# Kernel tuning notes

Hardware: AMD Instinct MI355X
Metric: run time of the kernel (lower is better)

## Reference

```python
import jax, jax.numpy as jnp
import numpy as np

HID = 128
MAX_NODES = 100000
MAX_EDGES = 300000
EVT_LEN = 4096
NUM_NODE = 20000
NUM_EDGE = 320000
# EVENT_TYPE_ID_MAP: pad=0 start=1 end=2 node-add=3 node-delete=4 edge-add=5 edge-delete=6
NODE_ADD, NODE_DEL = 3, 4


def time_encode(t, time_w, time_b):
    # TimeEncoder: cos(Linear(1 -> hidden)(t))
    return jnp.cos(t[..., None] * time_w + time_b)


def gru_cell(x, h, w_ih, w_hh, b_ih, b_hh):
    gi = x @ w_ih.T + b_ih
    gh = h @ w_hh.T + b_hh
    i_r, i_z, i_n = jnp.split(gi, 3, axis=-1)
    h_r, h_z, h_n = jnp.split(gh, 3, axis=-1)
    r = jax.nn.sigmoid(i_r + h_r)
    z = jax.nn.sigmoid(i_z + h_z)
    n = jnp.tanh(i_n + r * h_n)
    return (1.0 - z) * n + z * h


def setup_inputs() -> dict:
    key = jax.random.key(0)
    ks = jax.random.split(key, 32)
    H = HID
    s = 0.05
    inp = {}
    inp["event_type_ids"] = jax.random.randint(ks[0], (EVT_LEN,), 0, 7)
    inp["src_ids"] = jax.random.randint(ks[1], (EVT_LEN,), 0, MAX_NODES)
    inp["src_mask"] = (jax.random.uniform(ks[2], (EVT_LEN,)) > 0.3).astype(jnp.float32)
    inp["dst_ids"] = jax.random.randint(ks[3], (EVT_LEN,), 0, MAX_NODES)
    inp["dst_mask"] = (jax.random.uniform(ks[4], (EVT_LEN,)) > 0.3).astype(jnp.float32)
    inp["event_edge_ids"] = jax.random.randint(ks[5], (EVT_LEN,), 0, MAX_EDGES)
    inp["event_embeddings"] = jax.random.normal(ks[6], (EVT_LEN, H), dtype=jnp.float32)
    inp["event_mask"] = (jax.random.uniform(ks[7], (EVT_LEN,)) > 0.2).astype(jnp.float32)
    inp["event_timestamps"] = jax.random.uniform(ks[8], (EVT_LEN,)) * 100.0
    inp["node_ids"] = jax.random.randint(ks[9], (NUM_NODE,), 0, MAX_NODES)
    inp["edge_ids"] = jax.random.randint(ks[10], (NUM_EDGE,), 0, MAX_EDGES)
    inp["edge_index"] = jax.random.randint(ks[11], (2, NUM_EDGE), 0, NUM_NODE)
    inp["time"] = 100
    # persistent-buffer state
    inp["memory"] = jax.random.normal(ks[12], (MAX_NODES, H), dtype=jnp.float32) * s
    inp["last_update"] = jax.random.uniform(ks[13], (MAX_EDGES,)) * 50.0
    inp["node_features"] = jax.random.normal(ks[14], (MAX_NODES, H), dtype=jnp.float32) * s
    inp["edge_features"] = jax.random.normal(ks[15], (MAX_EDGES, H), dtype=jnp.float32) * s
    # TimeEncoder params (Linear(1, H))
    inp["time_w"] = jax.random.normal(ks[16], (H,), dtype=jnp.float32) * s
    inp["time_b"] = jax.random.normal(ks[17], (H,), dtype=jnp.float32) * s
    # GRUCell(5H -> H)
    inp["gru_w_ih"] = jax.random.normal(ks[18], (3 * H, 5 * H), dtype=jnp.float32) * s
    inp["gru_w_hh"] = jax.random.normal(ks[19], (3 * H, H), dtype=jnp.float32) * s
    inp["gru_b_ih"] = jax.random.normal(ks[20], (3 * H,), dtype=jnp.float32) * s
    inp["gru_b_hh"] = jax.random.normal(ks[21], (3 * H,), dtype=jnp.float32) * s
    # TransformerConv(H, H, heads=1, edge_dim=2H)
    inp["wq"] = jax.random.normal(ks[22], (H, H), dtype=jnp.float32) * s
    inp["bq"] = jax.random.normal(ks[23], (H,), dtype=jnp.float32) * s
    inp["wk"] = jax.random.normal(ks[24], (H, H), dtype=jnp.float32) * s
    inp["bk"] = jax.random.normal(ks[25], (H,), dtype=jnp.float32) * s
    inp["wv"] = jax.random.normal(ks[26], (H, H), dtype=jnp.float32) * s
    inp["bv"] = jax.random.normal(ks[27], (H,), dtype=jnp.float32) * s
    inp["we"] = jax.random.normal(ks[28], (H, 2 * H), dtype=jnp.float32) * s  # lin_edge, no bias
    inp["wskip"] = jax.random.normal(ks[29], (H, H), dtype=jnp.float32) * s
    inp["bskip"] = jax.random.normal(ks[30], (H,), dtype=jnp.float32) * s
    return inp


def reference(event_type_ids, src_ids, src_mask, dst_ids, dst_mask, event_edge_ids,
              event_embeddings, event_mask, event_timestamps, node_ids, edge_ids,
              edge_index, time, memory, last_update, node_features, edge_features,
              time_w, time_b, gru_w_ih, gru_w_hh, gru_b_ih, gru_b_hh,
              wq, bq, wk, bk, wv, bv, we, wskip, bskip):
    H = HID
    # ---- message() ----
    L = event_type_ids.shape[0]
    type_embs = jnp.broadcast_to(event_type_ids[:, None].astype(memory.dtype), (L, H))
    src_embs = memory[src_ids] * src_mask[:, None]
    dst_embs = memory[dst_ids] * dst_mask[:, None]
    edge_last = last_update[event_edge_ids]
    rel_ts = event_timestamps - edge_last * dst_mask
    is_node_ev = ((event_type_ids == NODE_ADD) | (event_type_ids == NODE_DEL)).astype(event_timestamps.dtype)
    ts_emb = time_encode(event_timestamps * is_node_ev + rel_ts * dst_mask, time_w, time_b) * event_mask[:, None]
    src_msgs = jnp.concatenate([type_embs, src_embs, dst_embs, ts_emb, event_embeddings], axis=1) * event_mask[:, None]
    dst_msgs = jnp.concatenate([type_embs, dst_embs, src_embs, ts_emb, event_embeddings], axis=1) * dst_mask[:, None]
    # ---- agg_message(): scatter-mean over node ids ----
    def agg(msgs, ids):
        s = jax.ops.segment_sum(msgs, ids, num_segments=MAX_NODES)
        c = jax.ops.segment_sum(jnp.ones((msgs.shape[0],), msgs.dtype), ids, num_segments=MAX_NODES)
        return s / jnp.maximum(c, 1.0)[:, None]
    agg_src = agg(src_msgs, src_ids)
    agg_dst = agg(dst_msgs, dst_ids)
    # ---- GRU memory update on unique ids ----
    # torch: memory[cat(uniq_src, uniq_dst)] = rnn(...); reads use pre-update memory,
    # dst writes come after src writes so they override on overlap. Duplicate ids in
    # src_ids carry identical per-id values, so scatter-set is equivalent to unique().
    new_src = gru_cell(agg_src[src_ids], memory[src_ids], gru_w_ih, gru_w_hh, gru_b_ih, gru_b_hh)
    new_dst = gru_cell(agg_dst[dst_ids], memory[dst_ids], gru_w_ih, gru_w_hh, gru_b_ih, gru_b_hh)
    memory = memory.at[src_ids].set(new_src)
    memory = memory.at[dst_ids].set(new_dst)
    # ---- edge attributes ----
    rel_t = time - last_update[edge_ids]
    rel_t_embs = time_encode(rel_t, time_w, time_b)
    edge_attr = jnp.concatenate([rel_t_embs, edge_features[edge_ids]], axis=-1)  # (E, 2H)
    # ---- TransformerConv (heads=1, concat, root_weight) ----
    x = node_features[node_ids] + memory[node_ids]  # (N, H)
    src, dst = edge_index[0], edge_index[1]
    q = x @ wq.T + bq
    k = x @ wk.T + bk
    v = x @ wv.T + bv
    e = edge_attr @ we.T  # lin_edge (no bias)
    alpha = jnp.sum(q[dst] * (k[src] + e), axis=-1) / jnp.sqrt(jnp.asarray(H, x.dtype))
    amax = jax.ops.segment_max(alpha, dst, num_segments=x.shape[0])
    ex = jnp.exp(alpha - amax[dst])
    denom = jax.ops.segment_sum(ex, dst, num_segments=x.shape[0])
    p = ex / jnp.maximum(denom[dst], 1e-16)
    out = jax.ops.segment_sum(p[:, None] * (v[src] + e), dst, num_segments=x.shape[0])
    return out + x @ wskip.T + bskip
```

## Files before the change

### kernel.cpp

```cpp
#include <hip/hip_runtime.h>
#include <math.h>

#define HID   128
#define MAXN  100000
#define MAXE  300000
#define EVT   4096
#define NNODE 20000
#define NEDGE 320000

typedef unsigned short u16;
typedef __attribute__((ext_vector_type(8))) short bf16x8;
typedef __attribute__((ext_vector_type(4))) float f32x4;

#define OFF_WIHB      0u
#define OFF_WHHB      491520u
#define OFF_WEB       589824u
#define OFF_WALLB     655360u
#define OFF_BALL      851968u
#define BASE2         855040u
#define OFF_REP_SRC   (BASE2 + 0u)
#define OFF_REP_DST   (BASE2 + 400128u)
#define OFF_CNT_SRC   (BASE2 + 800256u)
#define OFF_CNT_DST   (BASE2 + 1200384u)
#define OFF_SUM_SRC   (BASE2 + 1600512u)
#define OFF_SUM_DST   (BASE2 + 12086272u)
#define OFF_XGB       (BASE2 + 22572032u)
#define OFF_HG        (BASE2 + 33057792u)
#define OFF_HGB       (BASE2 + 37252096u)
#define OFF_GI        (BASE2 + 39349248u)
#define OFF_GH        (BASE2 + 51932160u)
#define OFF_NEWMEM    (BASE2 + 64515072u)
#define OFF_XB        (BASE2 + 0u)
#define OFF_QKVSE     (BASE2 + 5120000u)
#define OFF_KVB       (BASE2 + 66560000u)
#define OFF_DEG       (BASE2 + 76800000u)
#define OFF_OFFS      (BASE2 + 76880128u)
#define OFF_CURSOR    (BASE2 + 76960256u)
#define OFF_BSUM      (BASE2 + 77040384u)
#define OFF_SORTED    (BASE2 + 77041664u)
#define OFF_SACCB     (BASE2 + 78321664u)

__device__ __forceinline__ float sigmoidf_(float x) { return 1.f / (1.f + __expf(-x)); }
__device__ __forceinline__ u16 f2b(float f) {
    unsigned u = __float_as_uint(f);
    unsigned r = (u + 0x7fffu + ((u >> 16) & 1u)) >> 16;
    return (u16)r;
}
__device__ __forceinline__ float b2f(unsigned h) { return __uint_as_float(h << 16); }

__global__ void k_prep(const float* __restrict__ w_ih, const float* __restrict__ w_hh,
                       const float* __restrict__ we,
                       const float* __restrict__ wq, const float* __restrict__ wk_,
                       const float* __restrict__ wv, const float* __restrict__ wskip,
                       const float* __restrict__ bq, const float* __restrict__ bk,
                       const float* __restrict__ bv, const float* __restrict__ bskip,
                       u16* __restrict__ w_ih_b, u16* __restrict__ w_hh_b,
                       u16* __restrict__ we_b, u16* __restrict__ Wallb,
                       float* __restrict__ ball, int* __restrict__ deg) {
    int b = blockIdx.x, t = threadIdx.x;
    if (b < 960) {
        int i = b * 256 + t;
        w_ih_b[i] = f2b(w_ih[i]);
        return;
    }
    b -= 960;
    if (b < 192) {
        int i = b * 256 + t;
        w_hh_b[i] = f2b(w_hh[i]);
        return;
    }
    b -= 192;
    if (b < 128) {
        int i = b * 256 + t;
        we_b[i] = f2b(we[i]);
        return;
    }
    b -= 128;
    if (b < 79) {
        int i = b * 256 + t;
        if (i < NNODE) deg[i] = 0;
        return;
    }
    b -= 79;
    int idx = b * 256 + t;
    int row = idx >> 7;
    int k = idx & 127;
    float v;
    if (row < 128)      v = wq[row * 128 + k];
    else if (row < 256) v = wk_[(row - 128) * 128 + k];
    else if (row < 384) v = wv[(row - 256) * 128 + k];
    else if (row < 512) v = wskip[(row - 384) * 128 + k];
    else {
        int j = row - 512;
        float a = 0.f;
        for (int t2 = 0; t2 < 128; t2++) a += wq[t2 * 128 + k] * we[t2 * 256 + j];
        v = a;
    }
    Wallb[row * 128 + k] = f2b(v);
    if (k == 0) {
        float bb;
        if (row < 128)      bb = bq[row];
        else if (row < 256) bb = bk[row - 128];
        else if (row < 384) bb = bv[row - 256];
        else if (row < 512) bb = bskip[row - 384];
        else { int j = row - 512; float a = 0.f; for (int t2 = 0; t2 < 128; t2++) a += bq[t2] * we[t2 * 256 + j]; bb = a; }
        ball[row] = bb;
    }
}

__global__ void k_zero(char* __restrict__ base) {
    const int NFF = 50016;
    const int NZ  = 1360736;
    uint4 ff = make_uint4(0xFFFFFFFFu, 0xFFFFFFFFu, 0xFFFFFFFFu, 0xFFFFFFFFu);
    uint4 zz = make_uint4(0u, 0u, 0u, 0u);
    int idx = blockIdx.x * blockDim.x + threadIdx.x;
    int stride = gridDim.x * blockDim.x;
    uint4* pff = (uint4*)base;
    uint4* pzz = (uint4*)(base + 800256);
    for (int i = idx; i < NFF; i += stride) pff[i] = ff;
    for (int i = idx; i < NZ; i += stride) pzz[i] = zz;
}

__global__ void k_tables_deg(const int* __restrict__ src_ids, const int* __restrict__ dst_ids,
                             unsigned* rep_src, unsigned* rep_dst, int* cnt_src, int* cnt_dst,
                             const int* __restrict__ eidx, int* __restrict__ deg) {
    int b = blockIdx.x, t = threadIdx.x;
    if (b < 16) {
        int i = b * 256 + t;
        if (i >= EVT) return;
        int s = src_ids[i], d = dst_ids[i];
        atomicMin(&rep_src[s], (unsigned)i);
        atomicAdd(&cnt_src[s], 1);
        atomicMin(&rep_dst[d], (unsigned)i);
        atomicAdd(&cnt_dst[d], 1);
    } else {
        int j = (b - 16) * 256 + t;
        if (j >= NEDGE) return;
        atomicAdd(&deg[eidx[NEDGE + j]], 1);
    }
}

__global__ void k_message(const int* __restrict__ et_ids, const int* __restrict__ src_ids,
                          const float* __restrict__ src_mask, const int* __restrict__ dst_ids,
                          const float* __restrict__ dst_mask, const int* __restrict__ ev_eids,
                          const float* __restrict__ ev_emb, const float* __restrict__ ev_mask,
                          const float* __restrict__ ev_ts, const float* __restrict__ memory,
                          const float* __restrict__ last_update, const float* __restrict__ time_w,
                          const float* __restrict__ time_b, const unsigned* __restrict__ rep_src,
                          const unsigned* __restrict__ rep_dst, const int* __restrict__ cnt_src,
                          const int* __restrict__ cnt_dst, float* sum_src, float* sum_dst) {
    int i = blockIdx.x;
    int c = threadIdx.x;
    int et = et_ids[i];
    float sm = src_mask[i], dm = dst_mask[i], em = ev_mask[i], ts = ev_ts[i];
    int sid = src_ids[i], did = dst_ids[i], eid = ev_eids[i];
    float isnode = (et == 3 || et == 4) ? 1.f : 0.f;
    float rel = ts - last_update[eid] * dm;
    float tval = ts * isnode + rel * dm;
    float tse = __cosf(tval * time_w[c] + time_b[c]) * em;
    float typ = (float)et;
    float sv = memory[(size_t)sid * HID + c] * sm;
    float dv = memory[(size_t)did * HID + c] * dm;
    float ev = ev_emb[(size_t)i * HID + c];
    float* ps = sum_src + (size_t)rep_src[sid] * 640;
    if (cnt_src[sid] == 1) {
        ps[c] = typ * em; ps[128 + c] = sv * em; ps[256 + c] = dv * em;
        ps[384 + c] = tse * em; ps[512 + c] = ev * em;
    } else {
        atomicAdd(ps + c, typ * em);
        atomicAdd(ps + 128 + c, sv * em);
        atomicAdd(ps + 256 + c, dv * em);
        atomicAdd(ps + 384 + c, tse * em);
        atomicAdd(ps + 512 + c, ev * em);
    }
    float* pd = sum_dst + (size_t)rep_dst[did] * 640;
    if (cnt_dst[did] == 1) {
        pd[c] = typ * dm; pd[128 + c] = dv * dm; pd[256 + c] = sv * dm;
        pd[384 + c] = tse * dm; pd[512 + c] = ev * dm;
    } else {
        atomicAdd(pd + c, typ * dm);
        atomicAdd(pd + 128 + c, dv * dm);
        atomicAdd(pd + 256 + c, sv * dm);
        atomicAdd(pd + 384 + c, tse * dm);
        atomicAdd(pd + 512 + c, ev * dm);
    }
}

__global__ void k_build(const int* __restrict__ src_ids, const int* __restrict__ dst_ids,
                        const unsigned* __restrict__ rep_src, const unsigned* __restrict__ rep_dst,
                        const int* __restrict__ cnt_src, const int* __restrict__ cnt_dst,
                        const float* __restrict__ sum_src, const float* __restrict__ sum_dst,
                        const float* __restrict__ memory, u16* __restrict__ Xgb,
                        float* __restrict__ Hg, u16* __restrict__ Hgb) {
    int r = blockIdx.x, y = blockIdx.y, t = threadIdx.x;
    if (y == 5) {
        int id = (r < EVT) ? src_ids[r] : dst_ids[r - EVT];
        float v = memory[(size_t)id * HID + t];
        Hg[(size_t)r * HID + t] = v;
        Hgb[(size_t)r * HID + t] = f2b(v);
        return;
    }
    int c = y * 128 + t;
    float v;
    if (r < EVT) {
        int id = src_ids[r];
        int cnt = cnt_src[id]; if (cnt < 1) cnt = 1;
        v = sum_src[(size_t)rep_src[id] * 640 + c] / (float)cnt;
    } else {
        int id = dst_ids[r - EVT];
        int cnt = cnt_dst[id]; if (cnt < 1) cnt = 1;
        v = sum_dst[(size_t)rep_dst[id] * 640 + c] / (float)cnt;
    }
    Xgb[(size_t)r * 640 + c] = f2b(v);
}

__device__ __forceinline__ void gemm_tile(const u16* __restrict__ A, const u16* __restrict__ W,
                                          const float* __restrict__ bias, float* __restrict__ C,
                                          u16* __restrict__ KVb, int M, int N, int K, int acc,
                                          u16* Als, u16* Wls) {
    int tid = threadIdx.x;
    int bm = blockIdx.x * 128, bn = blockIdx.y * 128;
    int wave = tid >> 6, lane = tid & 63;
    int wm = (wave & 1) * 64, wn = (wave >> 1) * 64;
    int l15 = lane & 15, quad = lane >> 4;
    f32x4 accf[4][4] = {};
    for (int k0 = 0; k0 < K; k0 += 32) {
#pragma unroll
        for (int h = 0; h < 2; ++h) {
            int ch = tid + h * 256;
            int row = ch >> 2, kc = (ch & 3) * 8;
            int gr = bm + row;
            float4 av = make_float4(0.f, 0.f, 0.f, 0.f);
            if (gr < M) av = *(const float4*)(A + (size_t)gr * K + k0 + kc);
            *(float4*)&Als[row * 40 + kc] = av;
            int wr = bn + row;
            float4 wv_ = *(const float4*)(W + (size_t)wr * K + k0 + kc);
            *(float4*)&Wls[row * 40 + kc] = wv_;
        }
        __syncthreads();
        bf16x8 af[4], bfr[4];
#pragma unroll
        for (int r = 0; r < 4; ++r)
            af[r] = *(const bf16x8*)&Als[(wm + r * 16 + l15) * 40 + quad * 8];
#pragma unroll
        for (int c2 = 0; c2 < 4; ++c2)
            bfr[c2] = *(const bf16x8*)&Wls[(wn + c2 * 16 + l15) * 40 + quad * 8];
#pragma unroll
        for (int r = 0; r < 4; ++r)
#pragma unroll
            for (int c2 = 0; c2 < 4; ++c2)
                accf[r][c2] = __builtin_amdgcn_mfma_f32_16x16x32_bf16(af[r], bfr[c2], accf[r][c2], 0, 0, 0);
        __syncthreads();
    }
#pragma unroll
    for (int r = 0; r < 4; ++r) {
#pragma unroll
        for (int c2 = 0; c2 < 4; ++c2) {
            int ncol = bn + wn + c2 * 16 + l15;
            float bv = bias ? bias[ncol] : 0.f;
#pragma unroll
            for (int reg = 0; reg < 4; ++reg) {
                int mrow = bm + wm + r * 16 + quad * 4 + reg;
                if (mrow >= M) continue;
                float v = accf[r][c2][reg] + bv;
                if (KVb && ncol >= 128 && ncol < 384) {
                    KVb[(size_t)mrow * 256 + (ncol - 128)] = f2b(v);
                } else {
                    if (acc) v += C[(size_t)mrow * N + ncol];
                    C[(size_t)mrow * N + ncol] = v;
                }
            }
        }
    }
}

__global__ __launch_bounds__(256) void k_gemm_mfma(const u16* __restrict__ A,
                                                   const u16* __restrict__ W,
                                                   const float* __restrict__ bias,
                                                   float* __restrict__ C,
                                                   u16* __restrict__ KVb,
                                                   int M, int N, int K, int acc) {
    __shared__ u16 Als[128 * 40];
    __shared__ u16 Wls[128 * 40];
    gemm_tile(A, W, bias, C, KVb, M, N, K, acc, Als, Wls);
}

__global__ __launch_bounds__(256) void k_gemm_dual(const u16* __restrict__ A0, const u16* __restrict__ W0,
                                                   const float* __restrict__ b0, float* __restrict__ C0,
                                                   const u16* __restrict__ A1, const u16* __restrict__ W1,
                                                   const float* __restrict__ b1, float* __restrict__ C1) {
    __shared__ u16 Als[128 * 40];
    __shared__ u16 Wls[128 * 40];
    if (blockIdx.z == 0) gemm_tile(A0, W0, b0, C0, nullptr, 2 * EVT, 384, 640, 0, Als, Wls);
    else                 gemm_tile(A1, W1, b1, C1, nullptr, 2 * EVT, 384, 128, 0, Als, Wls);
}

__global__ void k_gru_scatter(const float* __restrict__ Gi, const float* __restrict__ Gh,
                              const float* __restrict__ Hg, const int* __restrict__ src_ids,
                              const int* __restrict__ dst_ids, const unsigned* __restrict__ rep_dst,
                              float* __restrict__ memory) {
    int r = blockIdx.x, c = threadIdx.x;
    const float* gi = Gi + (size_t)r * 384;
    const float* gh = Gh + (size_t)r * 384;
    float rg = sigmoidf_(gi[c] + gh[c]);
    float z  = sigmoidf_(gi[128 + c] + gh[128 + c]);
    float n  = tanhf(gi[256 + c] + rg * gh[256 + c]);
    float h0 = Hg[(size_t)r * HID + c];
    float h  = (1.f - z) * n + z * h0;
    if (r < EVT) {
        int sid = src_ids[r];
        if (rep_dst[sid] == 0xFFFFFFFFu) memory[(size_t)sid * HID + c] = h;
    } else {
        int did = dst_ids[r - EVT];
        memory[(size_t)did * HID + c] = h;
    }
}

__global__ void k_x(const int* __restrict__ node_ids, const float* __restrict__ nf,
                    const float* __restrict__ memory, u16* __restrict__ Xb) {
    int p = blockIdx.x, c = threadIdx.x;
    int nid = node_ids[p];
    Xb[(size_t)p * HID + c] = f2b(nf[(size_t)nid * HID + c] + memory[(size_t)nid * HID + c]);
}

__global__ __launch_bounds__(1024) void k_scan_one(const int* __restrict__ deg,
                                                   int* __restrict__ offs, int* __restrict__ cursor) {
    __shared__ int wsum[16];
    int t = threadIdx.x, lane = t & 63, w = t >> 6;
    int carry = 0;
    for (int base = 0; base < NNODE; base += 1024) {
        int i = base + t;
        int v = (i < NNODE) ? deg[i] : 0;
        int x = v;
#pragma unroll
        for (int d = 1; d < 64; d <<= 1) { int y = __shfl_up(x, d, 64); if (lane >= d) x += y; }
        if (lane == 63) wsum[w] = x;
        __syncthreads();
        int add = 0, tot = 0;
        for (int k2 = 0; k2 < 16; ++k2) { int s = wsum[k2]; if (k2 < w) add += s; tot += s; }
        if (i < NNODE) { int e = carry + add + x - v; offs[i] = e; cursor[i] = e; }
        carry += tot;
        __syncthreads();
    }
    if (t == 0) offs[NNODE] = NEDGE;
}

__global__ void k_sortscat(const int* __restrict__ eidx, int* __restrict__ cursor,
                           int* __restrict__ sorted) {
    int j = blockIdx.x * blockDim.x + threadIdx.x;
    if (j >= NEDGE) return;
    int d = eidx[NEDGE + j];
    int pos = atomicAdd(&cursor[d], 1);
    sorted[pos] = j;
}

__global__ __launch_bounds__(256) void k_node(const float* __restrict__ QK,
        const u16* __restrict__ KVb, const int* __restrict__ offs,
        const int* __restrict__ sorted, const int* __restrict__ eidx,
        const int* __restrict__ edge_ids, const float* __restrict__ last_update,
        const float* __restrict__ time_w, const float* __restrict__ time_b,
        const float* __restrict__ ef, const int* __restrict__ tptr,
        float* __restrict__ out, u16* __restrict__ saccb) {
    int wave = threadIdx.x >> 6, lane = threadIdx.x & 63;
    int n = blockIdx.x * 4 + wave;
    int c = 2 * lane;
    const float* base = QK + (size_t)n * 768;
    float2 qd   = *(const float2*)(base + c);
    float2 skip = *(const float2*)(base + 384 + c);
    float2 qet  = *(const float2*)(base + 512 + c);
    float2 qef  = *(const float2*)(base + 640 + c);
    float2 tw   = *(const float2*)(time_w + c);
    float2 tb   = *(const float2*)(time_b + c);
    float tf = (float)(*tptr);
    int start = offs[n], end = offs[n + 1];
    int deg = end - start;
    if (deg == 0) {
        *(float2*)(out + (size_t)n * HID + c) = skip;
        *(unsigned*)(saccb + (size_t)n * 256 + c) = 0u;
        *(unsigned*)(saccb + (size_t)n * 256 + 128 + c) = 0u;
        return;
    }
    float m = -1e30f, l_ = 0.f;
    float va0 = 0.f, va1 = 0.f, s00 = 0.f, s01 = 0.f, s10 = 0.f, s11 = 0.f;
    for (int cb = start; cb < end; cb += 64) {
        int cnt = end - cb; if (cnt > 64) cnt = 64;
        int s_l = 0, eid_l = 0; float rt_l = 0.f;
        if (lane < cnt) {
            int j = sorted[cb + lane];
            s_l = eidx[j];
            eid_l = edge_ids[j];
            rt_l = tf - last_update[eid_l];
        }
        for (int e0 = 0; e0 < cnt; e0 += 4) {
            float pv[4], cv0[4], cv1[4], vx[4], vy[4], ex[4], ey[4];
#pragma unroll
            for (int i = 0; i < 4; ++i) {
                int idx = e0 + i;
                int sel = (idx < cnt) ? idx : e0;
                int s   = __shfl(s_l, sel, 64);
                int eid = __shfl(eid_l, sel, 64);
                float rt = __shfl(rt_l, sel, 64);
                unsigned kvp = *(const unsigned*)(KVb + (size_t)s * 256 + c);
                unsigned vvp = *(const unsigned*)(KVb + (size_t)s * 256 + 128 + c);
                float2 ev = *(const float2*)(ef + (size_t)eid * HID + c);
                float k0f = b2f(kvp & 0xffffu), k1f = b2f(kvp >> 16);
                vx[i] = b2f(vvp & 0xffffu); vy[i] = b2f(vvp >> 16);
                cv0[i] = __cosf(rt * tw.x + tb.x);
                cv1[i] = __cosf(rt * tw.y + tb.y);
                ex[i] = ev.x; ey[i] = ev.y;
                pv[i] = qd.x * k0f + qd.y * k1f + qet.x * cv0[i] + qet.y * cv1[i]
                      + qef.x * ev.x + qef.y * ev.y;
            }
#pragma unroll
            for (int msk = 32; msk > 0; msk >>= 1) {
#pragma unroll
                for (int i = 0; i < 4; ++i) pv[i] += __shfl_xor(pv[i], msk, 64);
            }
            float al[4];
#pragma unroll
            for (int i = 0; i < 4; ++i)
                al[i] = (e0 + i < cnt) ? pv[i] * 0.08838834764831845f : -1e30f;
            float gm = fmaxf(fmaxf(al[0], al[1]), fmaxf(al[2], al[3]));
            if (gm > m) {
                float fac = __expf(m - gm);
                l_ *= fac; va0 *= fac; va1 *= fac;
                s00 *= fac; s01 *= fac; s10 *= fac; s11 *= fac;
                m = gm;
            }
#pragma unroll
            for (int i = 0; i < 4; ++i) {
                float w = __expf(al[i] - m);
                l_ += w;
                va0 += w * vx[i]; va1 += w * vy[i];
                s00 += w * cv0[i]; s01 += w * cv1[i];
                s10 += w * ex[i]; s11 += w * ey[i];
            }
        }
    }
    float inv = 1.f / fmaxf(l_, 1e-16f);
    float2 o; o.x = va0 * inv + skip.x; o.y = va1 * inv + skip.y;
    *(float2*)(out + (size_t)n * HID + c) = o;
    unsigned p0 = (unsigned)f2b(s00 * inv) | ((unsigned)f2b(s01 * inv) << 16);
    unsigned p1 = (unsigned)f2b(s10 * inv) | ((unsigned)f2b(s11 * inv) << 16);
    *(unsigned*)(saccb + (size_t)n * 256 + c) = p0;
    *(unsigned*)(saccb + (size_t)n * 256 + 128 + c) = p1;
}

extern "C" void kernel_launch(void* const* d_in, const int* in_sizes, int n_in,
                              void* d_out, int out_size, void* d_ws, size_t ws_size,
                              hipStream_t stream) {
    const int*   et_ids        = (const int*)d_in[0];
    const int*   src_ids       = (const int*)d_in[1];
    const float* src_mask      = (const float*)d_in[2];
    const int*   dst_ids       = (const int*)d_in[3];
    const float* dst_mask      = (const float*)d_in[4];
    const int*   ev_eids       = (const int*)d_in[5];
    const float* ev_emb        = (const float*)d_in[6];
    const float* ev_mask       = (const float*)d_in[7];
    const float* ev_ts         = (const float*)d_in[8];
    const int*   node_ids      = (const int*)d_in[9];
    const int*   edge_ids      = (const int*)d_in[10];
    const int*   edge_index    = (const int*)d_in[11];
    const int*   tptr          = (const int*)d_in[12];
    float*       memory        = (float*)d_in[13];
    const float* last_update   = (const float*)d_in[14];
    const float* node_features = (const float*)d_in[15];
    const float* edge_features = (const float*)d_in[16];
    const float* time_w        = (const float*)d_in[17];
    const float* time_b        = (const float*)d_in[18];
    const float* w_ih          = (const float*)d_in[19];
    const float* w_hh          = (const float*)d_in[20];
    const float* b_ih          = (const float*)d_in[21];
    const float* b_hh          = (const float*)d_in[22];
    const float* wq            = (const float*)d_in[23];
    const float* bq            = (const float*)d_in[24];
    const float* wk            = (const float*)d_in[25];
    const float* bk            = (const float*)d_in[26];
    const float* wv            = (const float*)d_in[27];
    const float* bv            = (const float*)d_in[28];
    const float* we            = (const float*)d_in[29];
    const float* wskip         = (const float*)d_in[30];
    const float* bskip         = (const float*)d_in[31];
    float* out = (float*)d_out;
    char*  wsb = (char*)d_ws;

    u16*   w_ih_b  = (u16*)(wsb + OFF_WIHB);
    u16*   w_hh_b  = (u16*)(wsb + OFF_WHHB);
    u16*   we_b    = (u16*)(wsb + OFF_WEB);
    u16*   Wallb   = (u16*)(wsb + OFF_WALLB);
    float* ball    = (float*)(wsb + OFF_BALL);
    unsigned* rep_src = (unsigned*)(wsb + OFF_REP_SRC);
    unsigned* rep_dst = (unsigned*)(wsb + OFF_REP_DST);
    int*   cnt_src = (int*)(wsb + OFF_CNT_SRC);
    int*   cnt_dst = (int*)(wsb + OFF_CNT_DST);
    float* sum_src = (float*)(wsb + OFF_SUM_SRC);
    float* sum_dst = (float*)(wsb + OFF_SUM_DST);
    u16*   Xgb     = (u16*)(wsb + OFF_XGB);
    float* Hg      = (float*)(wsb + OFF_HG);
    u16*   Hgb     = (u16*)(wsb + OFF_HGB);
    float* Gi      = (float*)(wsb + OFF_GI);
    float* Gh      = (float*)(wsb + OFF_GH);
    u16*   Xb      = (u16*)(wsb + OFF_XB);
    float* QKVSE   = (float*)(wsb + OFF_QKVSE);
    u16*   KVb     = (u16*)(wsb + OFF_KVB);
    int*   deg     = (int*)(wsb + OFF_DEG);
    int*   offs    = (int*)(wsb + OFF_OFFS);
    int*   cursor  = (int*)(wsb + OFF_CURSOR);
    int*   sorted  = (int*)(wsb + OFF_SORTED);
    u16*   saccb   = (u16*)(wsb + OFF_SACCB);

    k_prep<<<1743, 256, 0, stream>>>(w_ih, w_hh, we, wq, wk, wv, wskip, bq, bk, bv, bskip,
                                     w_ih_b, w_hh_b, we_b, Wallb, ball, deg);
    k_zero<<<2048, 256, 0, stream>>>(wsb + OFF_REP_SRC);
    k_tables_deg<<<1266, 256, 0, stream>>>(src_ids, dst_ids, rep_src, rep_dst, cnt_src, cnt_dst,
                                           edge_index, deg);
    k_message<<<EVT, 128, 0, stream>>>(et_ids, src_ids, src_mask, dst_ids, dst_mask, ev_eids,
                                       ev_emb, ev_mask, ev_ts, memory, last_update, time_w, time_b,
                                       rep_src, rep_dst, cnt_src, cnt_dst, sum_src, sum_dst);
    k_build<<<dim3(2 * EVT, 6), 128, 0, stream>>>(src_ids, dst_ids, rep_src, rep_dst,
                                                  cnt_src, cnt_dst, sum_src, sum_dst,
                                                  memory, Xgb, Hg, Hgb);
    k_gemm_dual<<<dim3(64, 3, 2), 256, 0, stream>>>(Xgb, w_ih_b, b_ih, Gi,
                                                    Hgb, w_hh_b, b_hh, Gh);
    k_gru_scatter<<<2 * EVT, 128, 0, stream>>>(Gi, Gh, Hg, src_ids, dst_ids, rep_dst, memory);

    k_x<<<NNODE, 128, 0, stream>>>(node_ids, node_features, memory, Xb);
    k_gemm_mfma<<<dim3(157, 6), 256, 0, stream>>>(Xb, Wallb, ball, QKVSE, KVb, NNODE, 768, 128, 0);
    k_scan_one<<<1, 1024, 0, stream>>>(deg, offs, cursor);
    k_sortscat<<<1250, 256, 0, stream>>>(edge_index, cursor, sorted);
    k_node<<<NNODE / 4, 256, 0, stream>>>(QKVSE, KVb, offs, sorted, edge_index, edge_ids,
                                          last_update, time_w, time_b, edge_features, tptr,
                                          out, saccb);
    k_gemm_mfma<<<dim3(157, 1), 256, 0, stream>>>(saccb, we_b, nullptr, out, nullptr, NNODE, 128, 256, 1);
}
```

Before: 535.2 us.

## Fuse zeroing into prep, build GRU inputs in message kernel, vectorize scan

Folds the workspace-zeroing kernel into the weight-prep launch as extra blocks. The message kernel now writes the bf16 GRU input rows and gathered memory rows directly. It keeps atomic accumulation only for node ids that occur more than once, and a small fix kernel rewrites those rows with the mean. This removes a launch and avoids reading the full sum buffers back for every row, at the cost of redundant Xgb writes for duplicate ids. The degree scan also processes four entries per thread with int4 loads and stores.

```diff
diff --git a/kernel.cpp b/kernel.cpp
--- a/kernel.cpp
+++ b/kernel.cpp
@@ -29,14 +29,12 @@
 #define OFF_HGB       (BASE2 + 37252096u)
 #define OFF_GI        (BASE2 + 39349248u)
 #define OFF_GH        (BASE2 + 51932160u)
-#define OFF_NEWMEM    (BASE2 + 64515072u)
 #define OFF_XB        (BASE2 + 0u)
 #define OFF_QKVSE     (BASE2 + 5120000u)
 #define OFF_KVB       (BASE2 + 66560000u)
 #define OFF_DEG       (BASE2 + 76800000u)
 #define OFF_OFFS      (BASE2 + 76880128u)
 #define OFF_CURSOR    (BASE2 + 76960256u)
-#define OFF_BSUM      (BASE2 + 77040384u)
 #define OFF_SORTED    (BASE2 + 77041664u)
 #define OFF_SACCB     (BASE2 + 78321664u)
 
@@ -56,7 +54,8 @@
                        const float* __restrict__ bv, const float* __restrict__ bskip,
                        u16* __restrict__ w_ih_b, u16* __restrict__ w_hh_b,
                        u16* __restrict__ we_b, u16* __restrict__ Wallb,
-                       float* __restrict__ ball, int* __restrict__ deg) {
+                       float* __restrict__ ball, int* __restrict__ deg,
+                       char* __restrict__ zbase) {
     int b = blockIdx.x, t = threadIdx.x;
     if (b < 960) {
         int i = b * 256 + t;
@@ -82,41 +81,42 @@
         return;
     }
     b -= 79;
-    int idx = b * 256 + t;
-    int row = idx >> 7;
-    int k = idx & 127;
-    float v;
-    if (row < 128)      v = wq[row * 128 + k];
-    else if (row < 256) v = wk_[(row - 128) * 128 + k];
-    else if (row < 384) v = wv[(row - 256) * 128 + k];
-    else if (row < 512) v = wskip[(row - 384) * 128 + k];
-    else {
-        int j = row - 512;
-        float a = 0.f;
-        for (int t2 = 0; t2 < 128; t2++) a += wq[t2 * 128 + k] * we[t2 * 256 + j];
-        v = a;
-    }
-    Wallb[row * 128 + k] = f2b(v);
-    if (k == 0) {
-        float bb;
-        if (row < 128)      bb = bq[row];
-        else if (row < 256) bb = bk[row - 128];
-        else if (row < 384) bb = bv[row - 256];
-        else if (row < 512) bb = bskip[row - 384];
-        else { int j = row - 512; float a = 0.f; for (int t2 = 0; t2 < 128; t2++) a += bq[t2] * we[t2 * 256 + j]; bb = a; }
-        ball[row] = bb;
-    }
-}
-
-__global__ void k_zero(char* __restrict__ base) {
+    if (b < 384) {
+        int idx = b * 256 + t;
+        int row = idx >> 7;
+        int k = idx & 127;
+        float v;
+        if (row < 128)      v = wq[row * 128 + k];
+        else if (row < 256) v = wk_[(row - 128) * 128 + k];
+        else if (row < 384) v = wv[(row - 256) * 128 + k];
+        else if (row < 512) v = wskip[(row - 384) * 128 + k];
+        else {
+            int j = row - 512;
+            float a = 0.f;
+            for (int t2 = 0; t2 < 128; t2++) a += wq[t2 * 128 + k] * we[t2 * 256 + j];
+            v = a;
+        }
+        Wallb[row * 128 + k] = f2b(v);
+        if (k == 0) {
+            float bb;
+            if (row < 128)      bb = bq[row];
+            else if (row < 256) bb = bk[row - 128];
+            else if (row < 384) bb = bv[row - 256];
+            else if (row < 512) bb = bskip[row - 384];
+            else { int j = row - 512; float a = 0.f; for (int t2 = 0; t2 < 128; t2++) a += bq[t2] * we[t2 * 256 + j]; bb = a; }
+            ball[row] = bb;
+        }
+        return;
+    }
+    b -= 384;
     const int NFF = 50016;
     const int NZ  = 1360736;
     uint4 ff = make_uint4(0xFFFFFFFFu, 0xFFFFFFFFu, 0xFFFFFFFFu, 0xFFFFFFFFu);
     uint4 zz = make_uint4(0u, 0u, 0u, 0u);
-    int idx = blockIdx.x * blockDim.x + threadIdx.x;
-    int stride = gridDim.x * blockDim.x;
-    uint4* pff = (uint4*)base;
-    uint4* pzz = (uint4*)(base + 800256);
+    int idx = b * 256 + t;
+    int stride = 1024 * 256;
+    uint4* pff = (uint4*)zbase;
+    uint4* pzz = (uint4*)(zbase + 800256);
     for (int i = idx; i < NFF; i += stride) pff[i] = ff;
     for (int i = idx; i < NZ; i += stride) pzz[i] = zz;
 }
@@ -148,7 +148,8 @@
                           const float* __restrict__ last_update, const float* __restrict__ time_w,
                           const float* __restrict__ time_b, const unsigned* __restrict__ rep_src,
                           const unsigned* __restrict__ rep_dst, const int* __restrict__ cnt_src,
-                          const int* __restrict__ cnt_dst, float* sum_src, float* sum_dst) {
+                          const int* __restrict__ cnt_dst, float* sum_src, float* sum_dst,
+                          u16* __restrict__ Xgb, float* __restrict__ Hg, u16* __restrict__ Hgb) {
     int i = blockIdx.x;
     int c = threadIdx.x;
     int et = et_ids[i];
@@ -159,59 +160,65 @@
     float tval = ts * isnode + rel * dm;
     float tse = __cosf(tval * time_w[c] + time_b[c]) * em;
     float typ = (float)et;
-    float sv = memory[(size_t)sid * HID + c] * sm;
-    float dv = memory[(size_t)did * HID + c] * dm;
+    float sv_raw = memory[(size_t)sid * HID + c];
+    float dv_raw = memory[(size_t)did * HID + c];
+    float sv = sv_raw * sm;
+    float dv = dv_raw * dm;
     float ev = ev_emb[(size_t)i * HID + c];
-    float* ps = sum_src + (size_t)rep_src[sid] * 640;
-    if (cnt_src[sid] == 1) {
-        ps[c] = typ * em; ps[128 + c] = sv * em; ps[256 + c] = dv * em;
-        ps[384 + c] = tse * em; ps[512 + c] = ev * em;
-    } else {
-        atomicAdd(ps + c, typ * em);
-        atomicAdd(ps + 128 + c, sv * em);
-        atomicAdd(ps + 256 + c, dv * em);
-        atomicAdd(ps + 384 + c, tse * em);
-        atomicAdd(ps + 512 + c, ev * em);
-    }
-    float* pd = sum_dst + (size_t)rep_dst[did] * 640;
-    if (cnt_dst[did] == 1) {
-        pd[c] = typ * dm; pd[128 + c] = dv * dm; pd[256 + c] = sv * dm;
-        pd[384 + c] = tse * dm; pd[512 + c] = ev * dm;
-    } else {
-        atomicAdd(pd + c, typ * dm);
-        atomicAdd(pd + 128 + c, dv * dm);
-        atomicAdd(pd + 256 + c, sv * dm);
-        atomicAdd(pd + 384 + c, tse * dm);
-        atomicAdd(pd + 512 + c, ev * dm);
-    }
-}
-
-__global__ void k_build(const int* __restrict__ src_ids, const int* __restrict__ dst_ids,
-                        const unsigned* __restrict__ rep_src, const unsigned* __restrict__ rep_dst,
-                        const int* __restrict__ cnt_src, const int* __restrict__ cnt_dst,
-                        const float* __restrict__ sum_src, const float* __restrict__ sum_dst,
-                        const float* __restrict__ memory, u16* __restrict__ Xgb,
-                        float* __restrict__ Hg, u16* __restrict__ Hgb) {
-    int r = blockIdx.x, y = blockIdx.y, t = threadIdx.x;
-    if (y == 5) {
-        int id = (r < EVT) ? src_ids[r] : dst_ids[r - EVT];
-        float v = memory[(size_t)id * HID + t];
-        Hg[(size_t)r * HID + t] = v;
-        Hgb[(size_t)r * HID + t] = f2b(v);
-        return;
-    }
-    int c = y * 128 + t;
-    float v;
+    Hg[(size_t)i * HID + c] = sv_raw;
+    Hgb[(size_t)i * HID + c] = f2b(sv_raw);
+    Hg[(size_t)(EVT + i) * HID + c] = dv_raw;
+    Hgb[(size_t)(EVT + i) * HID + c] = f2b(dv_raw);
+    float s0 = typ * em, s1 = sv * em, s2 = dv * em, s3 = tse * em, s4 = ev * em;
+    u16* xs = Xgb + (size_t)i * 640;
+    xs[c] = f2b(s0); xs[128 + c] = f2b(s1); xs[256 + c] = f2b(s2);
+    xs[384 + c] = f2b(s3); xs[512 + c] = f2b(s4);
+    if (cnt_src[sid] > 1) {
+        float* ps = sum_src + (size_t)rep_src[sid] * 640;
+        atomicAdd(ps + c, s0);
+        atomicAdd(ps + 128 + c, s1);
+        atomicAdd(ps + 256 + c, s2);
+        atomicAdd(ps + 384 + c, s3);
+        atomicAdd(ps + 512 + c, s4);
+    }
+    float d0 = typ * dm, d1 = dv * dm, d2 = sv * dm, d3 = tse * dm, d4 = ev * dm;
+    u16* xd = Xgb + (size_t)(EVT + i) * 640;
+    xd[c] = f2b(d0); xd[128 + c] = f2b(d1); xd[256 + c] = f2b(d2);
+    xd[384 + c] = f2b(d3); xd[512 + c] = f2b(d4);
+    if (cnt_dst[did] > 1) {
+        float* pd = sum_dst + (size_t)rep_dst[did] * 640;
+        atomicAdd(pd + c, d0);
+        atomicAdd(pd + 128 + c, d1);
+        atomicAdd(pd + 256 + c, d2);
+        atomicAdd(pd + 384 + c, d3);
+        atomicAdd(pd + 512 + c, d4);
+    }
+}
+
+__global__ void k_fix(const int* __restrict__ src_ids, const int* __restrict__ dst_ids,
+                      const unsigned* __restrict__ rep_src, const unsigned* __restrict__ rep_dst,
+                      const int* __restrict__ cnt_src, const int* __restrict__ cnt_dst,
+                      const float* __restrict__ sum_src, const float* __restrict__ sum_dst,
+                      u16* __restrict__ Xgb) {
+    int r = blockIdx.x, c = threadIdx.x;
+    const float* sum;
+    int cnt;
     if (r < EVT) {
         int id = src_ids[r];
-        int cnt = cnt_src[id]; if (cnt < 1) cnt = 1;
-        v = sum_src[(size_t)rep_src[id] * 640 + c] / (float)cnt;
+        cnt = cnt_src[id];
+        if (cnt < 2) return;
+        sum = sum_src + (size_t)rep_src[id] * 640;
     } else {
         int id = dst_ids[r - EVT];
-        int cnt = cnt_dst[id]; if (cnt < 1) cnt = 1;
-        v = sum_dst[(size_t)rep_dst[id] * 640 + c] / (float)cnt;
-    }
-    Xgb[(size_t)r * 640 + c] = f2b(v);
+        cnt = cnt_dst[id];
+        if (cnt < 2) return;
+        sum = sum_dst + (size_t)rep_dst[id] * 640;
+    }
+    float inv = 1.f / (float)cnt;
+    u16* x = Xgb + (size_t)r * 640;
+#pragma unroll
+    for (int y = 0; y < 5; ++y)
+        x[y * 128 + c] = f2b(sum[y * 128 + c] * inv);
 }
 
 __device__ __forceinline__ void gemm_tile(const u16* __restrict__ A, const u16* __restrict__ W,
@@ -328,17 +335,29 @@
     __shared__ int wsum[16];
     int t = threadIdx.x, lane = t & 63, w = t >> 6;
     int carry = 0;
-    for (int base = 0; base < NNODE; base += 1024) {
-        int i = base + t;
-        int v = (i < NNODE) ? deg[i] : 0;
-        int x = v;
+    const int N4 = NNODE / 4;
+    for (int base = 0; base < N4; base += 1024) {
+        int i4 = base + t;
+        int4 v = make_int4(0, 0, 0, 0);
+        if (i4 < N4) v = ((const int4*)deg)[i4];
+        int s = v.x + v.y + v.z + v.w;
+        int x = s;
 #pragma unroll
         for (int d = 1; d < 64; d <<= 1) { int y = __shfl_up(x, d, 64); if (lane >= d) x += y; }
         if (lane == 63) wsum[w] = x;
         __syncthreads();
         int add = 0, tot = 0;
-        for (int k2 = 0; k2 < 16; ++k2) { int s = wsum[k2]; if (k2 < w) add += s; tot += s; }
-        if (i < NNODE) { int e = carry + add + x - v; offs[i] = e; cursor[i] = e; }
+        for (int k2 = 0; k2 < 16; ++k2) { int ss = wsum[k2]; if (k2 < w) add += ss; tot += ss; }
+        if (i4 < N4) {
+            int e = carry + add + x - s;
+            int4 o;
+            o.x = e;
+            o.y = e + v.x;
+            o.z = o.y + v.y;
+            o.w = o.z + v.z;
+            ((int4*)offs)[i4] = o;
+            ((int4*)cursor)[i4] = o;
+        }
         carry += tot;
         __syncthreads();
     }
@@ -509,17 +528,16 @@
     int*   sorted  = (int*)(wsb + OFF_SORTED);
     u16*   saccb   = (u16*)(wsb + OFF_SACCB);
 
-    k_prep<<<1743, 256, 0, stream>>>(w_ih, w_hh, we, wq, wk, wv, wskip, bq, bk, bv, bskip,
-                                     w_ih_b, w_hh_b, we_b, Wallb, ball, deg);
-    k_zero<<<2048, 256, 0, stream>>>(wsb + OFF_REP_SRC);
+    k_prep<<<2767, 256, 0, stream>>>(w_ih, w_hh, we, wq, wk, wv, wskip, bq, bk, bv, bskip,
+                                     w_ih_b, w_hh_b, we_b, Wallb, ball, deg, wsb + OFF_REP_SRC);
     k_tables_deg<<<1266, 256, 0, stream>>>(src_ids, dst_ids, rep_src, rep_dst, cnt_src, cnt_dst,
                                            edge_index, deg);
     k_message<<<EVT, 128, 0, stream>>>(et_ids, src_ids, src_mask, dst_ids, dst_mask, ev_eids,
                                        ev_emb, ev_mask, ev_ts, memory, last_update, time_w, time_b,
-                                       rep_src, rep_dst, cnt_src, cnt_dst, sum_src, sum_dst);
-    k_build<<<dim3(2 * EVT, 6), 128, 0, stream>>>(src_ids, dst_ids, rep_src, rep_dst,
-                                                  cnt_src, cnt_dst, sum_src, sum_dst,
-                                                  memory, Xgb, Hg, Hgb);
+                                       rep_src, rep_dst, cnt_src, cnt_dst, sum_src, sum_dst,
+                                       Xgb, Hg, Hgb);
+    k_fix<<<2 * EVT, 128, 0, stream>>>(src_ids, dst_ids, rep_src, rep_dst,
+                                       cnt_src, cnt_dst, sum_src, sum_dst, Xgb);
     k_gemm_dual<<<dim3(64, 3, 2), 256, 0, stream>>>(Xgb, w_ih_b, b_ih, Gi,
                                                     Hgb, w_hh_b, b_hh, Gh);
     k_gru_scatter<<<2 * EVT, 128, 0, stream>>>(Gi, Gh, Hg, src_ids, dst_ids, rep_dst, memory);
```

After: 510.0 us. -4.7%, faster.
